# Optimization experiments

Hardware: AMD Instinct MI355X
Metric: run time of the kernel (lower is better)

Reference implementation:

```python
import jax, jax.numpy as jnp
import numpy as np

D_MODEL, N_HEADS, N_LEVELS, N_POINTS = 256, 8, 3, 4
HW = [(100, 152), (50, 76), (25, 38)]
S_TOTAL = sum(h * w for h, w in HW)  # 19950
B = 4


def _bilinear_sample(img, gx, gy, H, W):
    # img: [N, H*W, D]; gx, gy: [N, M] normalized coords in [-1, 1]
    # grid_sample semantics: align_corners=False, padding_mode='zeros'
    ix = (gx + 1.0) * 0.5 * W - 0.5
    iy = (gy + 1.0) * 0.5 * H - 0.5
    x0 = jnp.floor(ix)
    y0 = jnp.floor(iy)
    wx1 = ix - x0
    wy1 = iy - y0

    def corner(xc, yc, w):
        valid = (xc >= 0) & (xc < W) & (yc >= 0) & (yc < H)
        idx = (jnp.clip(yc, 0, H - 1) * W + jnp.clip(xc, 0, W - 1)).astype(jnp.int32)
        vals = jnp.take_along_axis(img, idx[:, :, None], axis=1)  # [N, M, D]
        return vals * (w * valid.astype(img.dtype))[:, :, None]

    return (corner(x0, y0, (1 - wx1) * (1 - wy1))
            + corner(x0 + 1, y0, wx1 * (1 - wy1))
            + corner(x0, y0 + 1, (1 - wx1) * wy1)
            + corner(x0 + 1, y0 + 1, wx1 * wy1))


def setup_inputs() -> dict:
    key = jax.random.key(0)
    ks = jax.random.split(key, 10)
    C = D_MODEL
    sc = 1.0 / np.sqrt(C)
    query = jax.random.normal(ks[0], (B, S_TOTAL, C), jnp.float32)
    value = jax.random.normal(ks[1], (B, S_TOTAL, C), jnp.float32)
    reference_points = jax.random.uniform(ks[2], (B, S_TOTAL, 2), jnp.float32)
    spatial_shapes = np.array(HW, dtype=np.int64)
    sizes = [h * w for h, w in HW]
    level_start_index = np.concatenate([[0], np.cumsum(sizes)[:-1]]).astype(np.int64)
    # Small offset weights keep sampled locations mostly in-bounds (as after training)
    W_off = jax.random.normal(ks[3], (N_HEADS * N_LEVELS * N_POINTS * 2, C), jnp.float32) * 0.01
    b_off = jax.random.normal(ks[4], (N_HEADS * N_LEVELS * N_POINTS * 2,), jnp.float32)
    W_attn = jax.random.normal(ks[5], (N_HEADS * N_LEVELS * N_POINTS, C), jnp.float32) * sc
    b_attn = jnp.zeros((N_HEADS * N_LEVELS * N_POINTS,), jnp.float32)
    W_val = jax.random.normal(ks[6], (C, C), jnp.float32) * sc
    b_val = jnp.zeros((C,), jnp.float32)
    W_out = jax.random.normal(ks[7], (C, C), jnp.float32) * sc
    b_out = jnp.zeros((C,), jnp.float32)
    return {"query": query, "value": value, "spatial_shapes": spatial_shapes,
            "level_start_index": level_start_index, "reference_points": reference_points,
            "W_off": W_off, "b_off": b_off, "W_attn": W_attn, "b_attn": b_attn,
            "W_val": W_val, "b_val": b_val, "W_out": W_out, "b_out": b_out}


def reference(query, value, spatial_shapes, level_start_index, reference_points,
              W_off, b_off, W_attn, b_attn, W_val, b_val, W_out, b_out):
    Bq, S, C = query.shape
    Dh = C // N_HEADS
    ss = np.asarray(spatial_shapes)          # static [L,2] (H,W)
    lsi = np.asarray(level_start_index)      # static [L]

    v = (value @ W_val.T + b_val).reshape(Bq, S, N_HEADS, Dh)
    off = (query @ W_off.T + b_off).reshape(Bq, S, N_HEADS, N_LEVELS, N_POINTS, 2)
    attn = jax.nn.softmax(
        (query @ W_attn.T + b_attn).reshape(Bq, S, N_HEADS, N_LEVELS, N_POINTS), axis=-1)

    # normalizer per level: (W, H) to normalize (x, y) offsets
    normalizer = jnp.asarray(ss[:, ::-1].astype(np.float32))  # [L, 2]
    ref = reference_points[:, :, None, None, None, :]          # [B,S,1,1,1,2]
    loc = ref + off / normalizer[None, None, None, :, None, :]  # [B,S,H,L,P,2]

    out = jnp.zeros((Bq, S, N_HEADS, Dh), query.dtype)
    for lvl in range(N_LEVELS):
        H, W = int(ss[lvl, 0]), int(ss[lvl, 1])
        start = int(lsi[lvl])
        # value for this level: [B*Hn, H*W, Dh]
        v_l = v[:, start:start + H * W].transpose(0, 2, 1, 3).reshape(Bq * N_HEADS, H * W, Dh)
        g = loc[:, :, :, lvl] * 2.0 - 1.0                      # [B,S,Hn,P,2]
        g = g.transpose(0, 2, 1, 3, 4).reshape(Bq * N_HEADS, S * N_POINTS, 2)
        sampled = _bilinear_sample(v_l, g[..., 0], g[..., 1], H, W)  # [B*Hn, S*P, Dh]
        sampled = sampled.reshape(Bq, N_HEADS, S, N_POINTS, Dh)
        w_l = attn[:, :, :, lvl].transpose(0, 2, 1, 3)         # [B,Hn,S,P]
        out = out + jnp.einsum('bhspd,bhsp->bshd', sampled, w_l)
    return out.reshape(Bq, S, C) @ W_out.T + b_out
```

## Files before the change

kernel.cpp:

```cpp
#include <hip/hip_runtime.h>

typedef unsigned short u16;
typedef unsigned int u32;
typedef __attribute__((ext_vector_type(8))) short short8v;
typedef __attribute__((ext_vector_type(4))) float f32x4;
typedef __attribute__((ext_vector_type(2))) float f32x2;
typedef __attribute__((ext_vector_type(4))) unsigned int uint4v;
typedef __attribute__((ext_vector_type(2))) unsigned int uint2v;
typedef __attribute__((ext_vector_type(8))) unsigned short us8;
typedef __attribute__((ext_vector_type(4))) unsigned short us4;

#define B_   4
#define S_   19950
#define C_   256
#define NH   8
#define DH   32
#define BS_  (B_*S_)

#define BM 64
#define BN 128
#define BK 64
#define NPAN 1248

__device__ __forceinline__ float bf2f(u16 u){ u32 x=((u32)u)<<16; float f; __builtin_memcpy(&f,&x,4); return f; }
__device__ __forceinline__ u16 f2bf(float f){ u32 x; __builtin_memcpy(&x,&f,4); x += 0x7fffu + ((x>>16)&1u); return (u16)(x>>16); }
__device__ __forceinline__ u32 cvtpk(float a, float b){ u32 r; asm("v_cvt_pk_bf16_f32 %0, %1, %2" : "=v"(r) : "v"(a), "v"(b)); return r; }
__device__ __forceinline__ f32x2 pkfma(f32x2 a, f32x2 b, f32x2 d){
  asm("v_pk_fma_f32 %0, %1, %2, %0" : "+v"(d) : "v"(a), "v"(b)); return d;
}
__device__ __forceinline__ f32x2 unpk(u32 p){
  uint2v u; u.x = p<<16; u.y = p & 0xffff0000u; return __builtin_bit_cast(f32x2, u);
}

template<int MODE>
__device__ __forceinline__ void gemm_core(int g, u32* smem,
    const void* __restrict__ Aany, const float* __restrict__ Wmain,
    const float* __restrict__ Wattn, const float* __restrict__ bmain,
    const float* __restrict__ battn, void* __restrict__ out0, u16* __restrict__ out1)
{
  constexpr int NX = (MODE==1) ? 3 : 2;
  float* Asf = (float*)smem;
  u16*  Asb  = (u16*)smem;
  u32*  Bs   = smem + ((MODE==2) ? 2048 : 4096);

  const int tid = threadIdx.x;
  const int x = (g>>3) % NX;
  const int y = ((g>>3)/NX)*8 + (g&7);
  const int m0 = y * BM;
  const int n0 = x * BN;
  const int lane = tid & 63;
  const int wid  = tid >> 6;
  const int wm = wid >> 1, wn = wid & 1;
  const int ln15 = lane & 15, ln4 = lane >> 4;

  f32x4 acc[2][4];
  #pragma unroll
  for (int i=0;i<2;++i){
    #pragma unroll
    for (int j=0;j<4;++j) acc[i][j] = (f32x4){0.f,0.f,0.f,0.f};
  }

  f32x4 bvv[8];
  auto loadB = [&](int k0){
    #pragma unroll
    for (int i=0;i<8;++i){
      const int ct = tid + 256*i;
      const int row = ct >> 4, c = ct & 15;
      const int n = n0 + row;
      f32x4 vv = (f32x4){0.f,0.f,0.f,0.f};
      if constexpr (MODE==1) {
        if (n < 192)      vv = *(const f32x4*)(Wmain + (size_t)n*C_ + k0 + c*4);
        else if (n < 288) vv = *(const f32x4*)(Wattn + (size_t)(n-192)*C_ + k0 + c*4);
      } else {
        vv = *(const f32x4*)(Wmain + (size_t)n*C_ + k0 + c*4);
      }
      bvv[i] = vv;
    }
  };

  loadB(0);

  #pragma unroll
  for (int kt=0; kt<4; ++kt) {
    const int k0 = kt*BK;
    if constexpr (MODE==2) {
      const u16* Ab = (const u16*)Aany;
      #pragma unroll
      for (int i=0;i<2;++i){
        const int rl = wid*16 + i*8 + (lane>>3);
        const int rg = min(m0 + rl, BS_-1);
        const int c = lane & 7, cs = c ^ (rl & 7);
        __builtin_amdgcn_global_load_lds(Ab + (size_t)rg*C_ + k0 + cs*8,
            &Asb[(wid*16 + i*8)*64], 16, 0, 0);
      }
    } else {
      const float* Ab = (const float*)Aany;
      #pragma unroll
      for (int i=0;i<4;++i){
        const int rl = wid*16 + i*4 + (lane>>4);
        const int rg = min(m0 + rl, BS_-1);
        const int c = lane & 15, cs = c ^ (rl & 15);
        __builtin_amdgcn_global_load_lds(Ab + (size_t)rg*C_ + k0 + cs*4,
            &Asf[(wid*16 + i*4)*64], 16, 0, 0);
      }
    }
    __builtin_amdgcn_sched_barrier(0);
    #pragma unroll
    for (int i=0;i<8;++i){
      const int ct = tid + 256*i;
      const int row = ct >> 4, c = ct & 15;
      const u32 p0 = cvtpk(bvv[i].x, bvv[i].y), p1 = cvtpk(bvv[i].z, bvv[i].w);
      const int cc = c >> 1;
      uint2v pk; pk.x = p0; pk.y = p1;
      *(uint2v*)&Bs[row*32 + ((cc ^ (row&7))<<2) + (c&1)*2] = pk;
    }
    if (kt < 3) {
      loadB(k0 + BK);
      asm volatile("s_waitcnt vmcnt(8) lgkmcnt(0)" ::: "memory");
    } else {
      asm volatile("s_waitcnt vmcnt(0) lgkmcnt(0)" ::: "memory");
    }
    __builtin_amdgcn_s_barrier();
    __builtin_amdgcn_sched_barrier(0);
    #pragma unroll
    for (int ks=0; ks<2; ++ks) {
      short8v af[2], bfr[4];
      #pragma unroll
      for (int mi=0;mi<2;++mi){
        const int row = wm*32 + mi*16 + ln15;
        if constexpr (MODE==2) {
          const int c = ks*4 + ln4;
          af[mi] = *(const short8v*)&Asb[row*64 + ((c ^ (row&7))<<3)];
        } else {
          const int ch = ks*8 + ln4*2;
          const int c1 = ch ^ (row&15), c2 = (ch+1) ^ (row&15);
          const f32x4 lo = *(const f32x4*)&Asf[row*64 + c1*4];
          const f32x4 hi = *(const f32x4*)&Asf[row*64 + c2*4];
          uint4v uu;
          uu.x = cvtpk(lo.x, lo.y); uu.y = cvtpk(lo.z, lo.w);
          uu.z = cvtpk(hi.x, hi.y); uu.w = cvtpk(hi.z, hi.w);
          af[mi] = __builtin_bit_cast(short8v, uu);
        }
      }
      #pragma unroll
      for (int ni=0;ni<4;++ni){
        const int row = wn*64 + ni*16 + ln15;
        const int c = ks*4 + ln4;
        bfr[ni] = *(const short8v*)&Bs[row*32 + ((c ^ (row&7))<<2)];
      }
      #pragma unroll
      for (int mi=0;mi<2;++mi){
        #pragma unroll
        for (int ni=0;ni<4;++ni)
          acc[mi][ni] = __builtin_amdgcn_mfma_f32_16x16x32_bf16(af[mi], bfr[ni], acc[mi][ni], 0, 0, 0);
      }
    }
    __syncthreads();
  }

  if constexpr (MODE==2) {
    float* Cs = (float*)smem;
    float* outp = (float*)out0;
    #pragma unroll
    for (int p=0;p<2;++p){
      if (wm == p) {
        #pragma unroll
        for (int mi=0;mi<2;++mi){
          #pragma unroll
          for (int ni=0;ni<4;++ni){
            const int col = wn*64 + ni*16 + ln15;
            const float bv = bmain[n0 + col];
            #pragma unroll
            for (int j=0;j<4;++j){
              const int rl = mi*16 + ln4*4 + j;
              Cs[rl*132 + col] = acc[mi][ni][j] + bv;
            }
          }
        }
      }
      __syncthreads();
      #pragma unroll
      for (int i=0;i<4;++i){
        const int c = i*256 + tid;
        const int row = c >> 5, ch = c & 31;
        const int m = m0 + p*32 + row;
        if (m < BS_) {
          const f32x4 vv = *(const f32x4*)&Cs[row*132 + ch*4];
          *(f32x4*)(outp + (size_t)m*C_ + n0 + ch*4) = vv;
        }
      }
      __syncthreads();
    }
  } else {
    u16* Cs = (u16*)smem;
    #pragma unroll
    for (int mi=0;mi<2;++mi){
      #pragma unroll
      for (int ni=0;ni<4;++ni){
        const int col = wn*64 + ni*16 + ln15;
        const int n = n0 + col;
        if (MODE==1 && n >= 288) continue;
        float bias;
        if constexpr (MODE==1) bias = (n < 192) ? bmain[n] : battn[n-192];
        else                   bias = bmain[n];
        if (MODE==1 && n >= 192) {
          #pragma unroll
          for (int j=0;j<4;++j){
            const int row = wm*32 + mi*16 + ln4*4 + j;
            const float vv = acc[mi][ni][j] + bias;
            float mx = vv;
            mx = fmaxf(mx, __shfl_xor(mx, 1));
            mx = fmaxf(mx, __shfl_xor(mx, 2));
            const float e = __expf(vv - mx);
            float ssum = e;
            ssum += __shfl_xor(ssum, 1);
            ssum += __shfl_xor(ssum, 2);
            Cs[row*136 + col] = f2bf(e/ssum);
          }
        } else {
          #pragma unroll
          for (int j=0;j<4;++j){
            const int row = wm*32 + mi*16 + ln4*4 + j;
            Cs[row*136 + col] = f2bf(acc[mi][ni][j] + bias);
          }
        }
      }
    }
    __syncthreads();
    #pragma unroll
    for (int i=0;i<4;++i){
      const int c = i*256 + tid;
      const int row = c >> 4, ch = c & 15;
      const int m = m0 + row;
      if (m >= BS_) continue;
      const int colg = n0 + ch*8;
      const int bq = m / S_, sq = m - bq*S_;
      if constexpr (MODE==0) {
        const uint4v vv = *(const uint4v*)&Cs[row*136 + ch*8];
        u16* vout = (u16*)out0;
        const int h = colg >> 5, dh0 = colg & 31;
        *(uint4v*)(vout + ((size_t)(bq*NH+h)*S_ + sq)*DH + dh0) = vv;
      } else {
        if (colg < 192) {
          const uint4v vv = *(const uint4v*)&Cs[row*136 + ch*8];
          u16* soff = (u16*)out0;
          const int hh = colg / 24, cc = colg - hh*24;
          *(uint4v*)(soff + (((size_t)hh*4 + bq)*S_ + sq)*24 + cc) = vv;
        } else if (colg < 288) {
          #pragma unroll
          for (int half=0; half<2; ++half){
            const int nl2 = colg + half*4 - 192;
            const int hh = nl2 / 12, cc = nl2 - hh*12;
            const uint2v vv = *(const uint2v*)&Cs[row*136 + ch*8 + half*4];
            *(uint2v*)(out1 + (((size_t)hh*4 + bq)*S_ + sq)*12 + cc) = vv;
          }
        }
      }
    }
  }
}

__global__ __launch_bounds__(256) void k_projF(
    const void* __restrict__ value, const float* __restrict__ Wv,
    const float* __restrict__ bv, void* __restrict__ vout,
    const void* __restrict__ query, const float* __restrict__ Wo,
    const float* __restrict__ Wa, const float* __restrict__ bo,
    const float* __restrict__ ba, void* __restrict__ soff, u16* __restrict__ sattn)
{
  __shared__ u32 smem[8192];
  const int g = blockIdx.x;
  if (g < 2*NPAN) gemm_core<0>(g,          smem, value, Wv, nullptr, bv, nullptr, vout, nullptr);
  else            gemm_core<1>(g - 2*NPAN, smem, query, Wo, Wa,      bo, ba,      soff, sattn);
}

__global__ __launch_bounds__(256) void k_gemm2F(const void* __restrict__ A,
    const float* __restrict__ W, const float* __restrict__ b, void* __restrict__ o)
{
  __shared__ u32 smem[6144];
  gemm_core<2>(blockIdx.x, smem, A, W, nullptr, b, nullptr, o, nullptr);
}

#define NCH 312

__global__ __launch_bounds__(256) void k_sample7(const u16* __restrict__ v,
    const u16* __restrict__ soff, const u16* __restrict__ sattn,
    const float* __restrict__ refp, u16* __restrict__ tmp)
{
  const int g = blockIdx.x;
  const int xcd = g & 7, inner = g >> 3;
  const int unit = inner / NCH;
  const int cidx = inner - unit*NCH;
  const int bh = xcd*4 + unit;
  const int b = bh >> 3, h = bh & 7;
  const int dh0 = (threadIdx.x & 3) * 8;
  const int q = cidx*64 + (threadIdx.x >> 2);
  if (q >= S_) return;
  const size_t r = (size_t)b*S_ + q;
  const float refx = refp[r*2+0], refy = refp[r*2+1];
  const char* vb = (const char*)(v + (size_t)bh * S_ * DH);

  const u16* sop = soff + (((size_t)h*4 + b)*S_ + q)*24;
  const u16* sap = sattn + (((size_t)h*4 + b)*S_ + q)*12;
  us8 so0 = *(const us8*)(sop);
  us8 so1 = *(const us8*)(sop + 8);
  us8 so2 = *(const us8*)(sop + 16);
  us4 sa0 = *(const us4*)(sap);
  us4 sa1 = *(const us4*)(sap + 4);
  us4 sa2 = *(const us4*)(sap + 8);
  u16 soarr[24]; u16 saarr[12];
  #pragma unroll
  for (int i=0;i<8;++i){ soarr[i]=so0[i]; soarr[8+i]=so1[i]; soarr[16+i]=so2[i]; }
  #pragma unroll
  for (int i=0;i<4;++i){ saarr[i]=sa0[i]; saarr[4+i]=sa1[i]; saarr[8+i]=sa2[i]; }

  f32x2 acc0 = (f32x2){0.f,0.f}, acc1 = acc0, acc2 = acc0, acc3 = acc0;
  const int WLs[3]={152,76,38}, HLs[3]={100,50,25}, STs[3]={0,15200,19000};
  const u32 ch2 = (u32)(dh0*2);
  #pragma unroll
  for (int l=0;l<3;++l) {
    const int Wl=WLs[l], Hl=HLs[l];
    const float rxl = refx*(float)Wl - 0.5f;
    const float ryl = refy*(float)Hl - 0.5f;
    const char* vbl = vb + (size_t)STs[l]*DH*2;
    #pragma unroll
    for (int p=0;p<4;++p) {
      const int idx = l*4 + p;
      const float ix = rxl + bf2f(soarr[2*idx+0]);
      const float iy = ryl + bf2f(soarr[2*idx+1]);
      const float aw = bf2f(saarr[idx]);
      const float x0f = floorf(ix), y0f = floorf(iy);
      const float wx1 = ix-x0f, wy1 = iy-y0f;
      const int x0 = (int)x0f, y0 = (int)y0f;
      const int x1 = x0+1, y1 = y0+1;
      const float wx0z = ((u32)x0 < (u32)Wl) ? (1.f-wx1) : 0.f;
      const float wx1z = ((u32)x1 < (u32)Wl) ? wx1 : 0.f;
      const float wy0z = ((u32)y0 < (u32)Hl) ? aw*(1.f-wy1) : 0.f;
      const float wy1z = ((u32)y1 < (u32)Hl) ? aw*wy1 : 0.f;
      const int xi0 = min(max(x0,0),Wl-1), xi1 = min(max(x1,0),Wl-1);
      const int yi0 = min(max(y0,0),Hl-1), yi1 = min(max(y1,0),Hl-1);
      const u32 rb0 = (u32)(yi0*Wl)*64u + ch2;
      const u32 rb1 = (u32)(yi1*Wl)*64u + ch2;
      const uint4v t00 = *(const uint4v*)(vbl + rb0 + (u32)xi0*64u);
      const uint4v t01 = *(const uint4v*)(vbl + rb0 + (u32)xi1*64u);
      const uint4v t10 = *(const uint4v*)(vbl + rb1 + (u32)xi0*64u);
      const uint4v t11 = *(const uint4v*)(vbl + rb1 + (u32)xi1*64u);
      const float w00 = wx0z*wy0z, w01 = wx1z*wy0z;
      const float w10 = wx0z*wy1z, w11 = wx1z*wy1z;
      f32x2 W00 = (f32x2){w00,w00}, W01 = (f32x2){w01,w01};
      f32x2 W10 = (f32x2){w10,w10}, W11 = (f32x2){w11,w11};
      acc0 = pkfma(unpk(t00.x), W00, acc0);
      acc1 = pkfma(unpk(t00.y), W00, acc1);
      acc2 = pkfma(unpk(t00.z), W00, acc2);
      acc3 = pkfma(unpk(t00.w), W00, acc3);
      acc0 = pkfma(unpk(t01.x), W01, acc0);
      acc1 = pkfma(unpk(t01.y), W01, acc1);
      acc2 = pkfma(unpk(t01.z), W01, acc2);
      acc3 = pkfma(unpk(t01.w), W01, acc3);
      acc0 = pkfma(unpk(t10.x), W10, acc0);
      acc1 = pkfma(unpk(t10.y), W10, acc1);
      acc2 = pkfma(unpk(t10.z), W10, acc2);
      acc3 = pkfma(unpk(t10.w), W10, acc3);
      acc0 = pkfma(unpk(t11.x), W11, acc0);
      acc1 = pkfma(unpk(t11.y), W11, acc1);
      acc2 = pkfma(unpk(t11.z), W11, acc2);
      acc3 = pkfma(unpk(t11.w), W11, acc3);
    }
  }
  uint4v o;
  o.x = cvtpk(acc0.x, acc0.y); o.y = cvtpk(acc1.x, acc1.y);
  o.z = cvtpk(acc2.x, acc2.y); o.w = cvtpk(acc3.x, acc3.y);
  *(uint4v*)(tmp + r*C_ + (size_t)h*DH + dh0) = o;
}

extern "C" void kernel_launch(void* const* d_in, const int* in_sizes, int n_in,
                              void* d_out, int out_size, void* d_ws, size_t ws_size,
                              hipStream_t stream) {
  (void)in_sizes; (void)n_in; (void)out_size; (void)ws_size;
  const float* query = (const float*)d_in[0];
  const float* value = (const float*)d_in[1];
  const float* refp  = (const float*)d_in[4];
  const float* W_off = (const float*)d_in[5];
  const float* b_off = (const float*)d_in[6];
  const float* W_attn= (const float*)d_in[7];
  const float* b_attn= (const float*)d_in[8];
  const float* W_val = (const float*)d_in[9];
  const float* b_val = (const float*)d_in[10];
  const float* W_out = (const float*)d_in[11];
  const float* b_out = (const float*)d_in[12];
  float* out = (float*)d_out;

  char* ws = (char*)d_ws;
  constexpr size_t V_BYTES    = (size_t)BS_*C_*2;
  constexpr size_t SOFF_BYTES = (size_t)BS_*24*NH*2;
  constexpr size_t SATTN_BYTES= (size_t)BS_*12*NH*2;
  u16* v     = (u16*)(ws);
  u16* soff  = (u16*)(ws + V_BYTES);
  u16* sattn = (u16*)(ws + V_BYTES + SOFF_BYTES);
  u16* tmp   = (u16*)(ws + V_BYTES + SOFF_BYTES + SATTN_BYTES);

  dim3 blk(256);
  hipLaunchKernelGGL(k_projF, dim3(5*NPAN), blk, 0, stream,
                     (const void*)value, W_val, b_val, (void*)v,
                     (const void*)query, W_off, W_attn, b_off, b_attn,
                     (void*)soff, sattn);
  hipLaunchKernelGGL(k_sample7, dim3(8*4*NCH), blk, 0, stream, v, soff, sattn, refp, tmp);
  hipLaunchKernelGGL(k_gemm2F, dim3(2*NPAN), blk, 0, stream,
                     (const void*)tmp, W_out, b_out, (void*)out);
}
```

Measured before the change: 241.1 us.

## Register-prefetch A tiles, convert to bf16 before LDS, shrink shared memory

Replaces direct global-to-LDS loads of the A tile with register prefetch of the next k-tile, converting fp32 activations to bf16 once before the LDS store rather than on every fragment read. The A tile now occupies half the LDS in fp32 modes, so k_projF's shared memory drops from 32KB to 24KB, which may allow more resident blocks. The trailing __syncthreads becomes a bare s_barrier, relying on explicit waitcnt handling. The cost is extra registers for the prefetched A data, and the first-tile writeA lambda is defined but never called (the loop inlines the same code).

New measurement: 257.3 us. 1.07x slower.

```diff
diff --git a/kernel.cpp b/kernel.cpp
--- a/kernel.cpp
+++ b/kernel.cpp
@@ -39,9 +39,8 @@
     const float* __restrict__ battn, void* __restrict__ out0, u16* __restrict__ out1)
 {
   constexpr int NX = (MODE==1) ? 3 : 2;
-  float* Asf = (float*)smem;
-  u16*  Asb  = (u16*)smem;
-  u32*  Bs   = smem + ((MODE==2) ? 2048 : 4096);
+  u16* As16 = (u16*)smem;
+  u32* Bs   = smem + 2048;
 
   const int tid = threadIdx.x;
   const int x = (g>>3) % NX;
@@ -59,6 +58,37 @@
     #pragma unroll
     for (int j=0;j<4;++j) acc[i][j] = (f32x4){0.f,0.f,0.f,0.f};
   }
+
+  const int ar = tid >> 2, ac = tid & 3;
+  const size_t aRow = (size_t)min(m0 + ar, BS_-1) * C_;
+  f32x4  avf[4];
+  uint4v avb[2];
+  auto loadA = [&](int k0){
+    if constexpr (MODE==2) {
+      const u16* Ab = (const u16*)Aany;
+      #pragma unroll
+      for (int j=0;j<2;++j) avb[j] = *(const uint4v*)(Ab + aRow + k0 + (ac*2+j)*8);
+    } else {
+      const float* Af = (const float*)Aany;
+      #pragma unroll
+      for (int j=0;j<4;++j) avf[j] = *(const f32x4*)(Af + aRow + k0 + ac*16 + j*4);
+    }
+  };
+  auto writeA = [&](){
+    #pragma unroll
+    for (int j=0;j<2;++j){
+      const int c = ac*2 + j;
+      uint4v pk;
+      if constexpr (MODE==2) pk = avb[j];
+      else {
+        pk.x = cvtpk(avf[2*j].x,   avf[2*j].y);
+        pk.y = cvtpk(avf[2*j].z,   avf[2*j].w);
+        pk.z = cvtpk(avf[2*j+1].x, avf[2*j+1].y);
+        pk.w = cvtpk(avf[2*j+1].z, avf[2*j+1].w);
+      }
+      *(uint4v*)&As16[ar*64 + ((c ^ (ar&7))<<3)] = pk;
+    }
+  };
 
   f32x4 bvv[8];
   auto loadB = [&](int k0){
@@ -78,33 +108,23 @@
     }
   };
 
-  loadB(0);
+  loadA(0); loadB(0);
 
   #pragma unroll
   for (int kt=0; kt<4; ++kt) {
-    const int k0 = kt*BK;
-    if constexpr (MODE==2) {
-      const u16* Ab = (const u16*)Aany;
-      #pragma unroll
-      for (int i=0;i<2;++i){
-        const int rl = wid*16 + i*8 + (lane>>3);
-        const int rg = min(m0 + rl, BS_-1);
-        const int c = lane & 7, cs = c ^ (rl & 7);
-        __builtin_amdgcn_global_load_lds(Ab + (size_t)rg*C_ + k0 + cs*8,
-            &Asb[(wid*16 + i*8)*64], 16, 0, 0);
-      }
-    } else {
-      const float* Ab = (const float*)Aany;
-      #pragma unroll
-      for (int i=0;i<4;++i){
-        const int rl = wid*16 + i*4 + (lane>>4);
-        const int rg = min(m0 + rl, BS_-1);
-        const int c = lane & 15, cs = c ^ (rl & 15);
-        __builtin_amdgcn_global_load_lds(Ab + (size_t)rg*C_ + k0 + cs*4,
-            &Asf[(wid*16 + i*4)*64], 16, 0, 0);
-      }
-    }
-    __builtin_amdgcn_sched_barrier(0);
+    #pragma unroll
+    for (int j=0;j<2;++j){
+      const int c = ac*2 + j;
+      uint4v pk;
+      if constexpr (MODE==2) pk = avb[j];
+      else {
+        pk.x = cvtpk(avf[2*j].x,   avf[2*j].y);
+        pk.y = cvtpk(avf[2*j].z,   avf[2*j].w);
+        pk.z = cvtpk(avf[2*j+1].x, avf[2*j+1].y);
+        pk.w = cvtpk(avf[2*j+1].z, avf[2*j+1].w);
+      }
+      *(uint4v*)&As16[ar*64 + ((c ^ (ar&7))<<3)] = pk;
+    }
     #pragma unroll
     for (int i=0;i<8;++i){
       const int ct = tid + 256*i;
@@ -114,12 +134,8 @@
       uint2v pk; pk.x = p0; pk.y = p1;
       *(uint2v*)&Bs[row*32 + ((cc ^ (row&7))<<2) + (c&1)*2] = pk;
     }
-    if (kt < 3) {
-      loadB(k0 + BK);
-      asm volatile("s_waitcnt vmcnt(8) lgkmcnt(0)" ::: "memory");
-    } else {
-      asm volatile("s_waitcnt vmcnt(0) lgkmcnt(0)" ::: "memory");
-    }
+    if (kt < 3) { loadA((kt+1)*BK); loadB((kt+1)*BK); }
+    asm volatile("s_waitcnt lgkmcnt(0)" ::: "memory");
     __builtin_amdgcn_s_barrier();
     __builtin_amdgcn_sched_barrier(0);
     #pragma unroll
@@ -128,19 +144,8 @@
       #pragma unroll
       for (int mi=0;mi<2;++mi){
         const int row = wm*32 + mi*16 + ln15;
-        if constexpr (MODE==2) {
-          const int c = ks*4 + ln4;
-          af[mi] = *(const short8v*)&Asb[row*64 + ((c ^ (row&7))<<3)];
-        } else {
-          const int ch = ks*8 + ln4*2;
-          const int c1 = ch ^ (row&15), c2 = (ch+1) ^ (row&15);
-          const f32x4 lo = *(const f32x4*)&Asf[row*64 + c1*4];
-          const f32x4 hi = *(const f32x4*)&Asf[row*64 + c2*4];
-          uint4v uu;
-          uu.x = cvtpk(lo.x, lo.y); uu.y = cvtpk(lo.z, lo.w);
-          uu.z = cvtpk(hi.x, hi.y); uu.w = cvtpk(hi.z, hi.w);
-          af[mi] = __builtin_bit_cast(short8v, uu);
-        }
+        const int c = ks*4 + ln4;
+        af[mi] = *(const short8v*)&As16[row*64 + ((c ^ (row&7))<<3)];
       }
       #pragma unroll
       for (int ni=0;ni<4;++ni){
@@ -155,7 +160,8 @@
           acc[mi][ni] = __builtin_amdgcn_mfma_f32_16x16x32_bf16(af[mi], bfr[ni], acc[mi][ni], 0, 0, 0);
       }
     }
-    __syncthreads();
+    __builtin_amdgcn_sched_barrier(0);
+    __builtin_amdgcn_s_barrier();
   }
 
   if constexpr (MODE==2) {
@@ -267,7 +273,7 @@
     const float* __restrict__ Wa, const float* __restrict__ bo,
     const float* __restrict__ ba, void* __restrict__ soff, u16* __restrict__ sattn)
 {
-  __shared__ u32 smem[8192];
+  __shared__ u32 smem[6144];
   const int g = blockIdx.x;
   if (g < 2*NPAN) gemm_core<0>(g,          smem, value, Wv, nullptr, bv, nullptr, vout, nullptr);
   else            gemm_core<1>(g - 2*NPAN, smem, query, Wo, Wa,      bo, ba,      soff, sattn);
```
